# Optimization experiments

Hardware: AMD Instinct MI355X
Metric: run time of the kernel (lower is better)

## Reference

```python
import jax, jax.numpy as jnp
import numpy as np

B, F, V, D_EMB = 16384, 32, 50000, 16
D_IN = F * D_EMB            # 512, concat embedding dim
N_TASK, N_SPEC, N_SH = 2, 2, 2
E = N_TASK * N_SPEC + N_SH  # 6 experts per CGC level
H1, H2 = 512, 256           # expert_params dims
T1, T2 = 128, 64            # tower dims


def setup_inputs() -> dict:
    key = jax.random.key(0)
    ks = iter(jax.random.split(key, 32))
    def w(shape, s=0.05):
        return jax.random.normal(next(ks), shape, jnp.float32) * s
    return dict(
        x_ids=jax.random.randint(next(ks), (B, F), 0, V),
        emb=w((F, V, D_EMB)),
        e1_W1=w((E, D_IN, H1)), e1_b1=jnp.zeros((E, H1), jnp.float32),
        e1_W2=w((E, H1, H2)), e1_b2=jnp.zeros((E, H2), jnp.float32),
        g1_Ws=w((N_TASK, D_IN, N_SPEC + N_SH)), g1_bs=jnp.zeros((N_TASK, N_SPEC + N_SH), jnp.float32),
        g1_Wsh=w((D_IN, E)), g1_bsh=jnp.zeros((E,), jnp.float32),
        e2_W1=w((E, H2, H1)), e2_b1=jnp.zeros((E, H1), jnp.float32),
        e2_W2=w((E, H1, H2)), e2_b2=jnp.zeros((E, H2), jnp.float32),
        g2_Ws=w((N_TASK, H2, N_SPEC + N_SH)), g2_bs=jnp.zeros((N_TASK, N_SPEC + N_SH), jnp.float32),
        tw_W1=w((N_TASK, H2, T1)), tw_b1=jnp.zeros((N_TASK, T1), jnp.float32),
        tw_W2=w((N_TASK, T1, T2)), tw_b2=jnp.zeros((N_TASK, T2), jnp.float32),
    )


def _cgc(x_list, W1, b1, W2, b2, Wg, bg, Wg_sh=None, bg_sh=None):
    # Stack expert inputs: task-t specific experts read x_list[t], shared read x_list[-1].
    X = jnp.stack([x_list[0]] * N_SPEC + [x_list[1]] * N_SPEC + [x_list[-1]] * N_SH)  # [E,B,Din]
    # Grouped two-layer expert MLP (BatchNorm is identity at eval-mode init).
    h = jax.nn.relu(jnp.einsum('ebd,edh->ebh', X, W1) + b1[:, None, :])   # [E,B,H1]
    out = jax.nn.relu(jnp.einsum('ebh,eho->ebo', h, W2) + b2[:, None, :])  # [E,B,H2]
    outs = []
    for t in range(N_TASK):
        gate = jax.nn.softmax(x_list[t] @ Wg[t] + bg[t], axis=-1)          # [B, N_SPEC+N_SH]
        sel = jnp.concatenate([out[t * N_SPEC:(t + 1) * N_SPEC], out[-N_SH:]], axis=0)
        outs.append(jnp.einsum('bk,kbo->bo', gate, sel))
    if Wg_sh is not None:  # shared gate only for levels < n_level
        gate = jax.nn.softmax(x_list[-1] @ Wg_sh + bg_sh, axis=-1)          # [B,E]
        outs.append(jnp.einsum('bk,kbo->bo', gate, out))
    return outs


def reference(x_ids, emb, e1_W1, e1_b1, e1_W2, e1_b2, g1_Ws, g1_bs, g1_Wsh, g1_bsh,
              e2_W1, e2_b1, e2_W2, e2_b2, g2_Ws, g2_bs, tw_W1, tw_b1, tw_W2, tw_b2):
    # Embedding lookup per sparse feature, then flatten (squeeze_dim=True).
    embed_x = emb[jnp.arange(F)[None, :], x_ids].reshape(B, D_IN)  # [B, 512]
    xs = [embed_x] * (N_TASK + 1)
    xs = _cgc(xs, e1_W1, e1_b1, e1_W2, e1_b2, g1_Ws, g1_bs, g1_Wsh, g1_bsh)  # level 1 -> 3 outs
    xs = _cgc(xs, e2_W1, e2_b1, e2_W2, e2_b2, g2_Ws, g2_bs)                  # level 2 -> 2 outs
    ys = []
    for t in range(N_TASK):
        h = jax.nn.relu(xs[t] @ tw_W1[t] + tw_b1[t])
        h = jax.nn.relu(h @ tw_W2[t] + tw_b2[t])
        ys.append(jax.nn.sigmoid(h))  # PredictionLayer('classification')
    return jnp.concatenate(ys, axis=1)  # [B, N_TASK*T2]
```

## Files before the change

### kernel.cpp

```cpp
#include <hip/hip_runtime.h>

typedef unsigned short u16;
typedef __attribute__((ext_vector_type(4))) unsigned short u16x4;
typedef __attribute__((ext_vector_type(8))) unsigned short u16x8;
typedef __attribute__((ext_vector_type(8))) short s16x8;
typedef __attribute__((ext_vector_type(4))) float f32x4;

#define BATCH 16384
#define NFEAT 32
#define NVOCAB 50000

__device__ __forceinline__ u16 f2bf(float f) {
    union { float f; unsigned u; } v; v.f = f;
    unsigned u = v.u;
    return (u16)((u + 0x7fffu + ((u >> 16) & 1u)) >> 16);
}
__device__ __forceinline__ float bf2f(u16 h) {
    union { unsigned u; float f; } v; v.u = ((unsigned)h) << 16;
    return v.f;
}

__device__ __forceinline__ void load_lds16(const u16* g, u16* l) {
    __builtin_amdgcn_global_load_lds(
        (const __attribute__((address_space(1))) void*)g,
        (__attribute__((address_space(3))) void*)l, 16, 0, 0);
}

struct PrepDesc { const float* src; u16* dst; int K; int N; int nz; int zbase; int frag; };
struct PrepArgs { PrepDesc d[6]; };

__global__ void prep_weights(PrepArgs args) {
    int z = blockIdx.z;
    int di = 0;
    #pragma unroll
    for (int i = 0; i < 6; i++)
        if (z >= args.d[i].zbase && z < args.d[i].zbase + args.d[i].nz) di = i;
    PrepDesc d = args.d[di];
    int zz = z - d.zbase;
    int k0 = blockIdx.x * 32, n0 = blockIdx.y * 32;
    if (k0 >= d.K || n0 >= d.N) return;
    __shared__ float tile[32][33];
    const float* src = d.src + (long)zz * d.K * d.N;
    u16* dst = d.dst + (long)zz * d.K * d.N;
    int tx = threadIdx.x & 31, ty = threadIdx.x >> 5;
    for (int r = ty; r < 32; r += 8) {
        int k = k0 + r, n = n0 + tx;
        tile[r][tx] = (k < d.K && n < d.N) ? src[(long)k * d.N + n] : 0.f;
    }
    __syncthreads();
    for (int r = ty; r < 32; r += 8) {
        int n = n0 + r, k = k0 + tx;
        if (n < d.N && k < d.K) {
            u16 v = f2bf(tile[tx][r]);
            if (d.frag) {
                long idx = (((long)(n >> 4) * (d.K >> 5) + (k >> 5)) * 4 + ((k >> 3) & 3)) * 128
                         + (long)(n & 15) * 8 + (k & 7);
                dst[idx] = v;
            } else {
                dst[(long)n * d.K + k] = v;
            }
        }
    }
}

__global__ void gather_embed(const int* __restrict__ ids,
                             const float* __restrict__ emb,
                             u16* __restrict__ out) {
    int idx = blockIdx.x * 256 + threadIdx.x;
    int d4 = idx & 3;
    int f  = (idx >> 2) & 31;
    int b  = idx >> 7;
    int id = ids[b * NFEAT + f];
    const float4* p = (const float4*)(emb + ((long)f * NVOCAB + id) * 16) + d4;
    float4 v = *p;
    u16x4 o;
    o.x = f2bf(v.x); o.y = f2bf(v.y); o.z = f2bf(v.z); o.w = f2bf(v.w);
    *(u16x4*)(out + (long)b * 512 + f * 16 + d4 * 4) = o;
}

struct FusedP {
    const u16* __restrict__ A; const u16* __restrict__ W1t; const float* __restrict__ b1;
    const u16* __restrict__ W2t; const float* __restrict__ b2; u16* __restrict__ O;
    int a_zshift; long a_zstride;
};

template<int NKT>
__device__ __forceinline__ void expert_impl(const FusedP p) {
    __shared__ u16 sA[64 * 64 * NKT];
    __shared__ u16 sH[64 * 128];
    const int K1 = NKT * 64;
    const int z = blockIdx.z;
    const int m0 = blockIdx.x * 64;
    const u16* Ab  = p.A + (long)(z >> p.a_zshift) * p.a_zstride;
    const u16* W1f = p.W1t + (long)z * 512 * K1;
    const u16* W2f = p.W2t + (long)z * 256 * 512;
    const int tid = threadIdx.x;
    const int lane = tid & 63;
    const int w = tid >> 6;
    const int l16 = lane & 15;
    const int q = lane >> 4;
    const int key = l16 & 7;

    const u16* W1l = W1f + q * 128 + l16 * 8;
    const u16* W2l = W2f + q * 128 + l16 * 8;

    const int tr = tid >> 3;
    const int lc = (tid & 7) ^ (tr & 7);
    const u16* gA0 = Ab + (long)(m0 + tr) * K1 + lc * 8;
    const int ldst = (tid & ~63) * 8;
    #pragma unroll
    for (int kt = 0; kt < NKT; ++kt) {
        #pragma unroll
        for (int i = 0; i < 2; ++i)
            load_lds16(gA0 + (long)(32 * i) * K1 + kt * 64, &sA[kt * 4096 + i * 2048 + ldst]);
    }
    __syncthreads();

    f32x4 acc[4][4] = {};

    #pragma unroll
    for (int c = 0; c < 4; ++c) {
        f32x4 acc1[4][2] = {};
        #pragma unroll 2
        for (int kt = 0; kt < NKT; ++kt) {
            #pragma unroll
            for (int kk = 0; kk < 2; ++kk) {
                const int pc = ((kk << 2) | q) ^ key;
                s16x8 af[4], bf[2];
                #pragma unroll
                for (int mt = 0; mt < 4; ++mt)
                    af[mt] = *(const s16x8*)(&sA[kt * 4096 + (mt * 16 + l16) * 64 + pc * 8]);
                #pragma unroll
                for (int nt = 0; nt < 2; ++nt) {
                    const int ntile = c * 8 + w * 2 + nt;
                    const int ks = kt * 2 + kk;
                    bf[nt] = *(const s16x8*)(W1l + (((long)ntile * (NKT * 2) + ks) << 9));
                }
                #pragma unroll
                for (int mt = 0; mt < 4; ++mt)
                    #pragma unroll
                    for (int nt = 0; nt < 2; ++nt)
                        acc1[mt][nt] = __builtin_amdgcn_mfma_f32_16x16x32_bf16(
                            bf[nt], af[mt], acc1[mt][nt], 0, 0, 0);
            }
        }
        __syncthreads();
        {
            const float* bb1 = p.b1 + (long)z * 512 + c * 128;
            #pragma unroll
            for (int mt = 0; mt < 4; ++mt) {
                int r = mt * 16 + l16;
                #pragma unroll
                for (int nt = 0; nt < 2; ++nt) {
                    int col = w * 32 + nt * 16 + q * 4;
                    float4 bv = *(const float4*)(bb1 + col);
                    f32x4 v = acc1[mt][nt];
                    u16x4 o;
                    o.x = f2bf(fmaxf(v.x + bv.x, 0.f));
                    o.y = f2bf(fmaxf(v.y + bv.y, 0.f));
                    o.z = f2bf(fmaxf(v.z + bv.z, 0.f));
                    o.w = f2bf(fmaxf(v.w + bv.w, 0.f));
                    int c8 = col >> 3;
                    *(u16x4*)(&sH[r * 128 + ((c8 ^ (r & 7)) << 3) + (q & 1) * 4]) = o;
                }
            }
        }
        __syncthreads();
        #pragma unroll
        for (int s = 0; s < 2; ++s) {
            #pragma unroll
            for (int kk = 0; kk < 2; ++kk) {
                const int kg = s * 8 + ((kk << 2) | q);
                s16x8 af[4], bf[4];
                #pragma unroll
                for (int mt = 0; mt < 4; ++mt) {
                    int r = mt * 16 + l16;
                    af[mt] = *(const s16x8*)(&sH[r * 128 + ((kg ^ key) << 3)]);
                }
                #pragma unroll
                for (int nt = 0; nt < 4; ++nt) {
                    const int ntile = w * 4 + nt;
                    const int ks2 = c * 4 + s * 2 + kk;
                    bf[nt] = *(const s16x8*)(W2l + (((long)ntile * 16 + ks2) << 9));
                }
                #pragma unroll
                for (int mt = 0; mt < 4; ++mt)
                    #pragma unroll
                    for (int nt = 0; nt < 4; ++nt)
                        acc[mt][nt] = __builtin_amdgcn_mfma_f32_16x16x32_bf16(
                            bf[nt], af[mt], acc[mt][nt], 0, 0, 0);
            }
        }
    }

    const float* bb2 = p.b2 + (long)z * 256;
    u16* Op = p.O + (long)z * BATCH * 256;
    #pragma unroll
    for (int mt = 0; mt < 4; ++mt) {
        int grow = m0 + mt * 16 + l16;
        u16* rowp = Op + (long)grow * 256;
        #pragma unroll
        for (int nt = 0; nt < 4; ++nt) {
            int gc = w * 64 + nt * 16 + q * 4;
            float4 bv = *(const float4*)(bb2 + gc);
            f32x4 v = acc[mt][nt];
            v.x = fmaxf(v.x + bv.x, 0.f);
            v.y = fmaxf(v.y + bv.y, 0.f);
            v.z = fmaxf(v.z + bv.z, 0.f);
            v.w = fmaxf(v.w + bv.w, 0.f);
            u16x4 o;
            o.x = f2bf(v.x); o.y = f2bf(v.y); o.z = f2bf(v.z); o.w = f2bf(v.w);
            *(u16x4*)(rowp + gc) = o;
        }
    }
}

__global__ __launch_bounds__(256, 2) void fused_l1(FusedP p) { expert_impl<8>(p); }
__global__ __launch_bounds__(256, 2) void fused_l2(FusedP p) { expert_impl<4>(p); }

__global__ __launch_bounds__(256, 1)
void tower_fused(const u16* __restrict__ x2, const u16* __restrict__ W1t,
                 const float* __restrict__ b1, const u16* __restrict__ W2t,
                 const float* __restrict__ b2, float* __restrict__ out) {
    const int t = blockIdx.y, m0 = blockIdx.x * 64;
    __shared__ u16 sX[64 * 256];
    __shared__ u16 sW1[128 * 256];
    __shared__ u16 sH[64 * 136];
    __shared__ u16 sW2[64 * 128];
    __shared__ float sB1[128];
    __shared__ float sB2[64];
    const int tid = threadIdx.x, lane = tid & 63, w = tid >> 6;
    const int l16 = lane & 15, q = lane >> 4;

    #pragma unroll
    for (int i = 0; i < 8; i++) {
        int c = i * 256 + tid, row = c >> 5, kc = c & 31;
        int lcc = (kc & ~7) | ((kc & 7) ^ (row & 7));
        load_lds16(x2 + ((long)t * BATCH + m0 + row) * 256 + lcc * 8,
                   &sX[(i * 256 + (tid & ~63)) * 8]);
    }
    #pragma unroll
    for (int i = 0; i < 16; i++) {
        int c = i * 256 + tid, row = c >> 5, kc = c & 31;
        int lcc = (kc & ~7) | ((kc & 7) ^ (row & 7));
        load_lds16(W1t + ((long)t * 128 + row) * 256 + lcc * 8,
                   &sW1[(i * 256 + (tid & ~63)) * 8]);
    }
    #pragma unroll
    for (int i = 0; i < 4; i++) {
        int c = i * 256 + tid, row = c >> 4, kc = c & 15;
        int lcc = (kc & ~7) | ((kc & 7) ^ (row & 7));
        load_lds16(W2t + ((long)t * 64 + row) * 128 + lcc * 8,
                   &sW2[(i * 256 + (tid & ~63)) * 8]);
    }
    if (tid < 128) sB1[tid] = b1[t * 128 + tid];
    if (tid < 64)  sB2[tid] = b2[t * 64 + tid];
    __syncthreads();

    f32x4 acc1[4][2] = {};
    #pragma unroll
    for (int kk = 0; kk < 8; kk++) {
        int pcb = kk * 4 + q;
        s16x8 af[4], bf[2];
        #pragma unroll
        for (int mt = 0; mt < 4; mt++) {
            int row = mt * 16 + l16;
            int sc = (pcb & ~7) | ((pcb & 7) ^ (row & 7));
            af[mt] = *(const s16x8*)(&sX[row * 256 + sc * 8]);
        }
        #pragma unroll
        for (int nt = 0; nt < 2; nt++) {
            int row = w * 32 + nt * 16 + l16;
            int sc = (pcb & ~7) | ((pcb & 7) ^ (row & 7));
            bf[nt] = *(const s16x8*)(&sW1[row * 256 + sc * 8]);
        }
        #pragma unroll
        for (int mt = 0; mt < 4; mt++)
            #pragma unroll
            for (int nt = 0; nt < 2; nt++)
                acc1[mt][nt] = __builtin_amdgcn_mfma_f32_16x16x32_bf16(
                    bf[nt], af[mt], acc1[mt][nt], 0, 0, 0);
    }
    #pragma unroll
    for (int mt = 0; mt < 4; mt++) {
        int row = mt * 16 + l16;
        #pragma unroll
        for (int nt = 0; nt < 2; nt++) {
            int col = w * 32 + nt * 16 + q * 4;
            f32x4 v = acc1[mt][nt];
            u16x4 o;
            o.x = f2bf(fmaxf(v.x + sB1[col + 0], 0.f));
            o.y = f2bf(fmaxf(v.y + sB1[col + 1], 0.f));
            o.z = f2bf(fmaxf(v.z + sB1[col + 2], 0.f));
            o.w = f2bf(fmaxf(v.w + sB1[col + 3], 0.f));
            *(u16x4*)(&sH[row * 136 + col]) = o;
        }
    }
    __syncthreads();

    f32x4 acc2[4] = {};
    #pragma unroll
    for (int kk = 0; kk < 4; kk++) {
        s16x8 af[4], bf;
        #pragma unroll
        for (int mt = 0; mt < 4; mt++) {
            int row = mt * 16 + l16;
            af[mt] = *(const s16x8*)(&sH[row * 136 + kk * 32 + q * 8]);
        }
        {
            int row = w * 16 + l16;
            int pc = kk * 4 + q;
            int sc = (pc & ~7) | ((pc & 7) ^ (row & 7));
            bf = *(const s16x8*)(&sW2[row * 128 + sc * 8]);
        }
        #pragma unroll
        for (int mt = 0; mt < 4; mt++)
            acc2[mt] = __builtin_amdgcn_mfma_f32_16x16x32_bf16(
                bf, af[mt], acc2[mt], 0, 0, 0);
    }
    #pragma unroll
    for (int mt = 0; mt < 4; mt++) {
        int grow = m0 + mt * 16 + l16;
        int col = w * 16 + q * 4;
        float4 bv = *(const float4*)(sB2 + col);
        f32x4 v = acc2[mt];
        float4 r;
        r.x = 1.f / (1.f + __expf(-(v.x + bv.x)));
        r.y = 1.f / (1.f + __expf(-(v.y + bv.y)));
        r.z = 1.f / (1.f + __expf(-(v.z + bv.z)));
        r.w = 1.f / (1.f + __expf(-(v.w + bv.w)));
        *(float4*)(out + (long)grow * 128 + t * 64 + col) = r;
    }
}

__global__ __launch_bounds__(256)
void gate1(const u16* __restrict__ embed, const u16* __restrict__ out1,
           const float* __restrict__ g1Ws, const float* __restrict__ g1bs,
           const float* __restrict__ gWsh, const float* __restrict__ gbsh,
           u16* __restrict__ x1) {
    const int m0 = blockIdx.x * 8;
    __shared__ float sg[8][16];
    const int tid = threadIdx.x;
    const int row = tid >> 5, l = tid & 31;
    const long rb = m0 + row;

    float a[4] = {0,0,0,0}, b[4] = {0,0,0,0}, c[6] = {0,0,0,0,0,0};
    {
        const u16* er = embed + rb * 512 + l * 16;
        u16x8 xa = *(const u16x8*)(er);
        u16x8 xb = *(const u16x8*)(er + 8);
        #pragma unroll
        for (int u = 0; u < 16; u++) {
            int k = l * 16 + u;
            float xv = bf2f(u < 8 ? xa[u] : xb[u - 8]);
            float4 wa = *(const float4*)(g1Ws + k * 4);
            float4 wb = *(const float4*)(g1Ws + 2048 + k * 4);
            a[0] += xv * wa.x; a[1] += xv * wa.y; a[2] += xv * wa.z; a[3] += xv * wa.w;
            b[0] += xv * wb.x; b[1] += xv * wb.y; b[2] += xv * wb.z; b[3] += xv * wb.w;
            float2 w0 = *(const float2*)(gWsh + k * 6);
            float2 w1 = *(const float2*)(gWsh + k * 6 + 2);
            float2 w2 = *(const float2*)(gWsh + k * 6 + 4);
            c[0] += xv * w0.x; c[1] += xv * w0.y;
            c[2] += xv * w1.x; c[3] += xv * w1.y;
            c[4] += xv * w2.x; c[5] += xv * w2.y;
        }
    }
    #pragma unroll
    for (int off = 1; off < 32; off <<= 1) {
        #pragma unroll
        for (int g = 0; g < 4; g++) { a[g] += __shfl_xor(a[g], off); b[g] += __shfl_xor(b[g], off); }
        #pragma unroll
        for (int g = 0; g < 6; g++) c[g] += __shfl_xor(c[g], off);
    }
    if (l == 0) {
        float mx, s, e[6];
        mx = -1e30f;
        for (int g = 0; g < 4; g++) { a[g] += g1bs[g]; mx = fmaxf(mx, a[g]); }
        s = 0.f; for (int g = 0; g < 4; g++) { e[g] = __expf(a[g] - mx); s += e[g]; }
        for (int g = 0; g < 4; g++) sg[row][g] = e[g] / s;
        mx = -1e30f;
        for (int g = 0; g < 4; g++) { b[g] += g1bs[4 + g]; mx = fmaxf(mx, b[g]); }
        s = 0.f; for (int g = 0; g < 4; g++) { e[g] = __expf(b[g] - mx); s += e[g]; }
        for (int g = 0; g < 4; g++) sg[row][4 + g] = e[g] / s;
        mx = -1e30f;
        for (int g = 0; g < 6; g++) { c[g] += gbsh[g]; mx = fmaxf(mx, c[g]); }
        s = 0.f; for (int g = 0; g < 6; g++) { e[g] = __expf(c[g] - mx); s += e[g]; }
        for (int g = 0; g < 6; g++) sg[row][8 + g] = e[g] / s;
    }
    __syncthreads();

    const int c8 = l * 8;
    const u16* ob = out1 + rb * 256 + c8;
    u16x8 o[6];
    #pragma unroll
    for (int k = 0; k < 6; k++) o[k] = *(const u16x8*)(ob + (long)k * BATCH * 256);
    const float* g = sg[row];
    u16x8 r0, r1, r2;
    #pragma unroll
    for (int u = 0; u < 8; u++) {
        float o0 = bf2f(o[0][u]), o1 = bf2f(o[1][u]), o2 = bf2f(o[2][u]);
        float o3 = bf2f(o[3][u]), o4 = bf2f(o[4][u]), o5 = bf2f(o[5][u]);
        r0[u] = f2bf(g[0] * o0 + g[1] * o1 + g[2] * o4 + g[3] * o5);
        r1[u] = f2bf(g[4] * o2 + g[5] * o3 + g[6] * o4 + g[7] * o5);
        r2[u] = f2bf(g[8] * o0 + g[9] * o1 + g[10] * o2 + g[11] * o3 + g[12] * o4 + g[13] * o5);
    }
    *(u16x8*)(x1 + ((long)0 * BATCH + rb) * 256 + c8) = r0;
    *(u16x8*)(x1 + ((long)1 * BATCH + rb) * 256 + c8) = r1;
    *(u16x8*)(x1 + ((long)2 * BATCH + rb) * 256 + c8) = r2;
}

__global__ __launch_bounds__(256)
void gate2(const u16* __restrict__ x1, const u16* __restrict__ out2,
           const float* __restrict__ g2Ws, const float* __restrict__ g2bs,
           u16* __restrict__ x2) {
    const int m0 = blockIdx.x * 8;
    __shared__ float sg[8][8];
    const int tid = threadIdx.x;
    const int row = tid >> 5, l = tid & 31;
    const long rb = m0 + row;

    float a[4] = {0,0,0,0}, b[4] = {0,0,0,0};
    {
        const u16* e0 = x1 + rb * 256 + l * 8;
        const u16* e1 = e0 + (long)BATCH * 256;
        u16x8 x0 = *(const u16x8*)e0;
        u16x8 x1v = *(const u16x8*)e1;
        #pragma unroll
        for (int u = 0; u < 8; u++) {
            int k = l * 8 + u;
            float4 wa = *(const float4*)(g2Ws + k * 4);
            float4 wb = *(const float4*)(g2Ws + 1024 + k * 4);
            float xv0 = bf2f(x0[u]), xv1 = bf2f(x1v[u]);
            a[0] += xv0 * wa.x; a[1] += xv0 * wa.y; a[2] += xv0 * wa.z; a[3] += xv0 * wa.w;
            b[0] += xv1 * wb.x; b[1] += xv1 * wb.y; b[2] += xv1 * wb.z; b[3] += xv1 * wb.w;
        }
    }
    #pragma unroll
    for (int off = 1; off < 32; off <<= 1) {
        #pragma unroll
        for (int g = 0; g < 4; g++) { a[g] += __shfl_xor(a[g], off); b[g] += __shfl_xor(b[g], off); }
    }
    if (l == 0) {
        float mx, s, e[4];
        mx = -1e30f;
        for (int g = 0; g < 4; g++) { a[g] += g2bs[g]; mx = fmaxf(mx, a[g]); }
        s = 0.f; for (int g = 0; g < 4; g++) { e[g] = __expf(a[g] - mx); s += e[g]; }
        for (int g = 0; g < 4; g++) sg[row][g] = e[g] / s;
        mx = -1e30f;
        for (int g = 0; g < 4; g++) { b[g] += g2bs[4 + g]; mx = fmaxf(mx, b[g]); }
        s = 0.f; for (int g = 0; g < 4; g++) { e[g] = __expf(b[g] - mx); s += e[g]; }
        for (int g = 0; g < 4; g++) sg[row][4 + g] = e[g] / s;
    }
    __syncthreads();

    const int c8 = l * 8;
    const u16* ob = out2 + rb * 256 + c8;
    u16x8 o[6];
    #pragma unroll
    for (int k = 0; k < 6; k++) o[k] = *(const u16x8*)(ob + (long)k * BATCH * 256);
    const float* g = sg[row];
    u16x8 r0, r1;
    #pragma unroll
    for (int u = 0; u < 8; u++) {
        float o0 = bf2f(o[0][u]), o1 = bf2f(o[1][u]), o2 = bf2f(o[2][u]);
        float o3 = bf2f(o[3][u]), o4 = bf2f(o[4][u]), o5 = bf2f(o[5][u]);
        r0[u] = f2bf(g[0] * o0 + g[1] * o1 + g[2] * o4 + g[3] * o5);
        r1[u] = f2bf(g[4] * o2 + g[5] * o3 + g[6] * o4 + g[7] * o5);
    }
    *(u16x8*)(x2 + ((long)0 * BATCH + rb) * 256 + c8) = r0;
    *(u16x8*)(x2 + ((long)1 * BATCH + rb) * 256 + c8) = r1;
}

extern "C" void kernel_launch(void* const* d_in, const int* in_sizes, int n_in,
                              void* d_out, int out_size, void* d_ws, size_t ws_size,
                              hipStream_t stream) {
    const int*   x_ids = (const int*)  d_in[0];
    const float* emb   = (const float*)d_in[1];
    const float* e1W1  = (const float*)d_in[2];
    const float* e1b1  = (const float*)d_in[3];
    const float* e1W2  = (const float*)d_in[4];
    const float* e1b2  = (const float*)d_in[5];
    const float* g1Ws  = (const float*)d_in[6];
    const float* g1bs  = (const float*)d_in[7];
    const float* g1Wsh = (const float*)d_in[8];
    const float* g1bsh = (const float*)d_in[9];
    const float* e2W1  = (const float*)d_in[10];
    const float* e2b1  = (const float*)d_in[11];
    const float* e2W2  = (const float*)d_in[12];
    const float* e2b2  = (const float*)d_in[13];
    const float* g2Ws  = (const float*)d_in[14];
    const float* g2bs  = (const float*)d_in[15];
    const float* twW1  = (const float*)d_in[16];
    const float* twb1  = (const float*)d_in[17];
    const float* twW2  = (const float*)d_in[18];
    const float* twb2  = (const float*)d_in[19];
    float* out = (float*)d_out;

    char* ws = (char*)d_ws;
    u16* embed   = (u16*)(ws + 0);
    u16* wt_e1W1 = (u16*)(ws + 16777216);
    u16* wt_e1W2 = (u16*)(ws + 19922944);
    u16* wt_e2W1 = (u16*)(ws + 21495808);
    u16* wt_e2W2 = (u16*)(ws + 23068672);
    u16* wt_twW1 = (u16*)(ws + 24641536);
    u16* wt_twW2 = (u16*)(ws + 24772608);
    u16* o_buf   = (u16*)(ws + 125468672);
    u16* x1      = (u16*)(ws + 175800320);
    u16* x2      = (u16*)(ws + 200966144);

    PrepArgs pa;
    pa.d[0] = { e1W1, wt_e1W1, 512, 512, 6,  0, 1 };
    pa.d[1] = { e1W2, wt_e1W2, 512, 256, 6,  6, 1 };
    pa.d[2] = { e2W1, wt_e2W1, 256, 512, 6, 12, 1 };
    pa.d[3] = { e2W2, wt_e2W2, 512, 256, 6, 18, 1 };
    pa.d[4] = { twW1, wt_twW1, 256, 128, 2, 24, 0 };
    pa.d[5] = { twW2, wt_twW2, 128,  64, 2, 26, 0 };
    prep_weights<<<dim3(16, 16, 28), 256, 0, stream>>>(pa);

    gather_embed<<<dim3(BATCH * NFEAT * 4 / 256), 256, 0, stream>>>(x_ids, emb, embed);

    FusedP f1 = { embed, wt_e1W1, e1b1, wt_e1W2, e1b2, o_buf, 3, 0L };
    fused_l1<<<dim3(BATCH / 64, 1, 6), 256, 0, stream>>>(f1);

    gate1<<<dim3(BATCH / 8), 256, 0, stream>>>(embed, o_buf, g1Ws, g1bs, g1Wsh, g1bsh, x1);

    FusedP f2 = { x1, wt_e2W1, e2b1, wt_e2W2, e2b2, o_buf, 1, (long)BATCH * 256 };
    fused_l2<<<dim3(BATCH / 64, 1, 6), 256, 0, stream>>>(f2);

    gate2<<<dim3(BATCH / 8), 256, 0, stream>>>(x1, o_buf, g2Ws, g2bs, x2);

    tower_fused<<<dim3(BATCH / 64, 2), 256, 0, stream>>>(x2, wt_twW1, twb1, wt_twW2, twb2, out);
}
```

Baseline: 562.5 us.

## Stage expert weights through LDS with 128-row tiles and 8 waves

The fused expert MLP kernels now use 128-row blocks with 512 threads (2x4 wave grid). Both the activation tile and the weight tiles for each k-step are staged in LDS with per-k-step barriers, instead of preloading all of A once and reading weight fragments straight from global memory. The fragment-permuted weight layout is dropped in favour of a plain transposed layout. The aim is to share each weight load across twice as many rows and make weight reads coalesced. The cost is many more barriers with no double buffering, so load latency is exposed, and the larger LDS footprint may limit occupancy.

```diff
diff --git a/kernel.cpp b/kernel.cpp
--- a/kernel.cpp
+++ b/kernel.cpp
@@ -26,7 +26,7 @@
         (__attribute__((address_space(3))) void*)l, 16, 0, 0);
 }
 
-struct PrepDesc { const float* src; u16* dst; int K; int N; int nz; int zbase; int frag; };
+struct PrepDesc { const float* src; u16* dst; int K; int N; int nz; int zbase; };
 struct PrepArgs { PrepDesc d[6]; };
 
 __global__ void prep_weights(PrepArgs args) {
@@ -50,16 +50,7 @@
     __syncthreads();
     for (int r = ty; r < 32; r += 8) {
         int n = n0 + r, k = k0 + tx;
-        if (n < d.N && k < d.K) {
-            u16 v = f2bf(tile[tx][r]);
-            if (d.frag) {
-                long idx = (((long)(n >> 4) * (d.K >> 5) + (k >> 5)) * 4 + ((k >> 3) & 3)) * 128
-                         + (long)(n & 15) * 8 + (k & 7);
-                dst[idx] = v;
-            } else {
-                dst[(long)n * d.K + k] = v;
-            }
-        }
+        if (n < d.N && k < d.K) dst[(long)n * d.K + k] = f2bf(tile[tx][r]);
     }
 }
 
@@ -79,63 +70,61 @@
 }
 
 struct FusedP {
-    const u16* __restrict__ A; const u16* __restrict__ W1t; const float* __restrict__ b1;
-    const u16* __restrict__ W2t; const float* __restrict__ b2; u16* __restrict__ O;
+    const u16* A; const u16* W1t; const float* b1;
+    const u16* W2t; const float* b2; u16* O;
     int a_zshift; long a_zstride;
 };
 
 template<int NKT>
 __device__ __forceinline__ void expert_impl(const FusedP p) {
-    __shared__ u16 sA[64 * 64 * NKT];
-    __shared__ u16 sH[64 * 128];
+    __shared__ u16 smem[32768];
+    u16* sA = smem;
+    u16* sH = smem;
+    u16* sW = smem + 16384;
     const int K1 = NKT * 64;
     const int z = blockIdx.z;
-    const int m0 = blockIdx.x * 64;
+    const int m0 = blockIdx.x * 128;
     const u16* Ab  = p.A + (long)(z >> p.a_zshift) * p.a_zstride;
-    const u16* W1f = p.W1t + (long)z * 512 * K1;
-    const u16* W2f = p.W2t + (long)z * 256 * 512;
+    const u16* W1b = p.W1t + (long)z * 512 * K1;
+    const u16* W2b = p.W2t + (long)z * 256 * 512;
     const int tid = threadIdx.x;
     const int lane = tid & 63;
     const int w = tid >> 6;
+    const int wm = w >> 2;
+    const int wn = w & 3;
     const int l16 = lane & 15;
     const int q = lane >> 4;
     const int key = l16 & 7;
-
-    const u16* W1l = W1f + q * 128 + l16 * 8;
-    const u16* W2l = W2f + q * 128 + l16 * 8;
 
     const int tr = tid >> 3;
     const int lc = (tid & 7) ^ (tr & 7);
     const u16* gA0 = Ab + (long)(m0 + tr) * K1 + lc * 8;
     const int ldst = (tid & ~63) * 8;
-    #pragma unroll
-    for (int kt = 0; kt < NKT; ++kt) {
-        #pragma unroll
-        for (int i = 0; i < 2; ++i)
-            load_lds16(gA0 + (long)(32 * i) * K1 + kt * 64, &sA[kt * 4096 + i * 2048 + ldst]);
-    }
-    __syncthreads();
 
     f32x4 acc[4][4] = {};
 
     #pragma unroll
     for (int c = 0; c < 4; ++c) {
         f32x4 acc1[4][2] = {};
-        #pragma unroll 2
         for (int kt = 0; kt < NKT; ++kt) {
+            __syncthreads();
+            load_lds16(gA0 + kt * 64,                  &sA[ldst]);
+            load_lds16(gA0 + (long)64 * K1 + kt * 64,  &sA[4096 + ldst]);
+            #pragma unroll
+            for (int i = 0; i < 2; ++i)
+                load_lds16(W1b + (long)(c * 128 + 64 * i + tr) * K1 + kt * 64 + lc * 8,
+                           &sW[i * 4096 + ldst]);
+            __syncthreads();
             #pragma unroll
             for (int kk = 0; kk < 2; ++kk) {
                 const int pc = ((kk << 2) | q) ^ key;
                 s16x8 af[4], bf[2];
                 #pragma unroll
                 for (int mt = 0; mt < 4; ++mt)
-                    af[mt] = *(const s16x8*)(&sA[kt * 4096 + (mt * 16 + l16) * 64 + pc * 8]);
-                #pragma unroll
-                for (int nt = 0; nt < 2; ++nt) {
-                    const int ntile = c * 8 + w * 2 + nt;
-                    const int ks = kt * 2 + kk;
-                    bf[nt] = *(const s16x8*)(W1l + (((long)ntile * (NKT * 2) + ks) << 9));
-                }
+                    af[mt] = *(const s16x8*)(&sA[(wm * 64 + mt * 16 + l16) * 64 + pc * 8]);
+                #pragma unroll
+                for (int nt = 0; nt < 2; ++nt)
+                    bf[nt] = *(const s16x8*)(&sW[(wn * 32 + nt * 16 + l16) * 64 + pc * 8]);
                 #pragma unroll
                 for (int mt = 0; mt < 4; ++mt)
                     #pragma unroll
@@ -149,10 +138,10 @@
             const float* bb1 = p.b1 + (long)z * 512 + c * 128;
             #pragma unroll
             for (int mt = 0; mt < 4; ++mt) {
-                int r = mt * 16 + l16;
+                int r = wm * 64 + mt * 16 + l16;
                 #pragma unroll
                 for (int nt = 0; nt < 2; ++nt) {
-                    int col = w * 32 + nt * 16 + q * 4;
+                    int col = wn * 32 + nt * 16 + q * 4;
                     float4 bv = *(const float4*)(bb1 + col);
                     f32x4 v = acc1[mt][nt];
                     u16x4 o;
@@ -160,29 +149,32 @@
                     o.y = f2bf(fmaxf(v.y + bv.y, 0.f));
                     o.z = f2bf(fmaxf(v.z + bv.z, 0.f));
                     o.w = f2bf(fmaxf(v.w + bv.w, 0.f));
-                    int c8 = col >> 3;
-                    *(u16x4*)(&sH[r * 128 + ((c8 ^ (r & 7)) << 3) + (q & 1) * 4]) = o;
+                    int grp = col >> 3;
+                    *(u16x4*)(&sH[r * 128 + ((grp ^ (r & 7)) << 3) + (q & 1) * 4]) = o;
                 }
             }
         }
-        __syncthreads();
         #pragma unroll
         for (int s = 0; s < 2; ++s) {
+            __syncthreads();
+            #pragma unroll
+            for (int i = 0; i < 4; ++i)
+                load_lds16(W2b + (long)(64 * i + tr) * 512 + c * 128 + s * 64 + lc * 8,
+                           &sW[i * 4096 + ldst]);
+            __syncthreads();
             #pragma unroll
             for (int kk = 0; kk < 2; ++kk) {
                 const int kg = s * 8 + ((kk << 2) | q);
+                const int pc = ((kk << 2) | q) ^ key;
                 s16x8 af[4], bf[4];
                 #pragma unroll
                 for (int mt = 0; mt < 4; ++mt) {
-                    int r = mt * 16 + l16;
+                    int r = wm * 64 + mt * 16 + l16;
                     af[mt] = *(const s16x8*)(&sH[r * 128 + ((kg ^ key) << 3)]);
                 }
                 #pragma unroll
-                for (int nt = 0; nt < 4; ++nt) {
-                    const int ntile = w * 4 + nt;
-                    const int ks2 = c * 4 + s * 2 + kk;
-                    bf[nt] = *(const s16x8*)(W2l + (((long)ntile * 16 + ks2) << 9));
-                }
+                for (int nt = 0; nt < 4; ++nt)
+                    bf[nt] = *(const s16x8*)(&sW[(wn * 64 + nt * 16 + l16) * 64 + pc * 8]);
                 #pragma unroll
                 for (int mt = 0; mt < 4; ++mt)
                     #pragma unroll
@@ -197,11 +189,11 @@
     u16* Op = p.O + (long)z * BATCH * 256;
     #pragma unroll
     for (int mt = 0; mt < 4; ++mt) {
-        int grow = m0 + mt * 16 + l16;
+        int grow = m0 + wm * 64 + mt * 16 + l16;
         u16* rowp = Op + (long)grow * 256;
         #pragma unroll
         for (int nt = 0; nt < 4; ++nt) {
-            int gc = w * 64 + nt * 16 + q * 4;
+            int gc = wn * 64 + nt * 16 + q * 4;
             float4 bv = *(const float4*)(bb2 + gc);
             f32x4 v = acc[mt][nt];
             v.x = fmaxf(v.x + bv.x, 0.f);
@@ -215,8 +207,8 @@
     }
 }
 
-__global__ __launch_bounds__(256, 2) void fused_l1(FusedP p) { expert_impl<8>(p); }
-__global__ __launch_bounds__(256, 2) void fused_l2(FusedP p) { expert_impl<4>(p); }
+__global__ __launch_bounds__(512, 2) void fused_l1(FusedP p) { expert_impl<8>(p); }
+__global__ __launch_bounds__(512, 2) void fused_l2(FusedP p) { expert_impl<4>(p); }
 
 __global__ __launch_bounds__(256, 1)
 void tower_fused(const u16* __restrict__ x2, const u16* __restrict__ W1t,
@@ -509,23 +501,23 @@
     u16* x2      = (u16*)(ws + 200966144);
 
     PrepArgs pa;
-    pa.d[0] = { e1W1, wt_e1W1, 512, 512, 6,  0, 1 };
-    pa.d[1] = { e1W2, wt_e1W2, 512, 256, 6,  6, 1 };
-    pa.d[2] = { e2W1, wt_e2W1, 256, 512, 6, 12, 1 };
-    pa.d[3] = { e2W2, wt_e2W2, 512, 256, 6, 18, 1 };
-    pa.d[4] = { twW1, wt_twW1, 256, 128, 2, 24, 0 };
-    pa.d[5] = { twW2, wt_twW2, 128,  64, 2, 26, 0 };
+    pa.d[0] = { e1W1, wt_e1W1, 512, 512, 6,  0 };
+    pa.d[1] = { e1W2, wt_e1W2, 512, 256, 6,  6 };
+    pa.d[2] = { e2W1, wt_e2W1, 256, 512, 6, 12 };
+    pa.d[3] = { e2W2, wt_e2W2, 512, 256, 6, 18 };
+    pa.d[4] = { twW1, wt_twW1, 256, 128, 2, 24 };
+    pa.d[5] = { twW2, wt_twW2, 128,  64, 2, 26 };
     prep_weights<<<dim3(16, 16, 28), 256, 0, stream>>>(pa);
 
     gather_embed<<<dim3(BATCH * NFEAT * 4 / 256), 256, 0, stream>>>(x_ids, emb, embed);
 
     FusedP f1 = { embed, wt_e1W1, e1b1, wt_e1W2, e1b2, o_buf, 3, 0L };
-    fused_l1<<<dim3(BATCH / 64, 1, 6), 256, 0, stream>>>(f1);
+    fused_l1<<<dim3(BATCH / 128, 1, 6), 512, 0, stream>>>(f1);
 
     gate1<<<dim3(BATCH / 8), 256, 0, stream>>>(embed, o_buf, g1Ws, g1bs, g1Wsh, g1bsh, x1);
 
     FusedP f2 = { x1, wt_e2W1, e2b1, wt_e2W2, e2b2, o_buf, 1, (long)BATCH * 256 };
-    fused_l2<<<dim3(BATCH / 64, 1, 6), 256, 0, stream>>>(f2);
+    fused_l2<<<dim3(BATCH / 128, 1, 6), 512, 0, stream>>>(f2);
 
     gate2<<<dim3(BATCH / 8), 256, 0, stream>>>(x1, o_buf, g2Ws, g2bs, x2);
 
```

Result: faster. 526.7 us (-6.4%).
